# Optimization experiments

Hardware: AMD Instinct MI355X
Metric: run time of the kernel (lower is better)

Reference implementation:

```python
import jax, jax.numpy as jnp
import numpy as np

BS, NX = 4, 4096
SD, NPAR, H, L, K = 2, 5, 128, 6, 16
DT = 0.1
EPS = 1e-5


def swish(x):
    return x * jax.nn.sigmoid(x)


def _gather(a, idx):
    # a: [bs, nx, F], idx: [bs, nx, k] -> [bs, nx, k, F]
    bs, nx, k = idx.shape
    flat = jnp.take_along_axis(a, idx.reshape(bs, nx * k)[:, :, None], axis=1)
    return flat.reshape(bs, nx, k, a.shape[-1])


def _knn_idx(pos, k):
    # pos: [bs, nx, sd] -> indices of k nearest neighbors (self excluded), [bs, nx, k]
    sq = jnp.sum(pos * pos, axis=-1)
    d2 = sq[:, :, None] + sq[:, None, :] - 2.0 * jnp.einsum('bnd,bmd->bnm', pos, pos)
    n = pos.shape[1]
    d2 = d2.at[:, jnp.arange(n), jnp.arange(n)].set(1e10)  # loop=False
    return jax.lax.top_k(-d2, k)[1]


def _instance_norm(x):
    # PyG InstanceNorm (affine=False): normalize per graph per channel over nodes
    m = jnp.mean(x, axis=1, keepdims=True)
    v = jnp.mean((x - m) ** 2, axis=1, keepdims=True)
    return (x - m) * jax.lax.rsqrt(v + EPS)


def _forward(inputs, case_params, grid, emb_w1, emb_b1, emb_w2, emb_b2,
             mw1, mb1, mw2, mb2, uw1, ub1, uw2, ub2, ow1, ob1, ow2, ob2):
    u = inputs[..., :1]  # var_id=0 slice (c==1 here)
    # per-batch, per-dim min-max normalization of grid -> pos in [0,1]
    gmin = jnp.min(grid, axis=1, keepdims=True)
    gmax = jnp.max(grid, axis=1, keepdims=True)
    pos = (grid - gmin) / (gmax - gmin)
    idx = _knn_idx(pos, K)  # [bs, nx, K]: neighbors j of each target i
    params = case_params

    f = swish(jnp.concatenate([u, pos, params], -1) @ emb_w1 + emb_b1)
    f = swish(f @ emb_w2 + emb_b2)

    u_j = _gather(u, idx)
    pos_j = _gather(pos, idx)
    du = u[:, :, None, :] - u_j       # u_i - u_j,   [bs,nx,K,1]
    dpos = pos[:, :, None, :] - pos_j  # pos_i - pos_j, [bs,nx,K,sd]
    var_i = jnp.broadcast_to(params[:, :, None, :], (BS, NX, K, NPAR))

    for l in range(L):
        f_j = _gather(f, idx)
        f_i = jnp.broadcast_to(f[:, :, None, :], f_j.shape)
        m = jnp.concatenate([f_i, f_j, du, dpos, var_i], -1)  # [bs,nx,K,2H+1+sd+npar]
        m = swish(m @ mw1[l] + mb1[l])
        m = swish(m @ mw2[l] + mb2[l])
        agg = jnp.mean(m, axis=2)  # mean aggregation over K incoming edges
        up = swish(jnp.concatenate([f, agg, params], -1) @ uw1[l] + ub1[l])
        up = swish(up @ uw2[l] + ub2[l])
        f = _instance_norm(f + up)  # residual (in==out) then InstanceNorm

    diff = swish(f @ ow1 + ob1) @ ow2 + ob2
    return u + DT * diff  # [bs, nx, 1]


def setup_inputs():
    key = jax.random.key(0)
    ks = jax.random.split(key, 16)
    s = 0.05
    d = {}
    d['inputs'] = jax.random.normal(ks[0], (BS, NX, 1), jnp.float32)
    d['case_params'] = jax.random.uniform(ks[1], (BS, NX, NPAR), dtype=jnp.float32)
    d['mask'] = jnp.ones((BS, NX, 1), jnp.float32)
    d['grid'] = jax.random.uniform(ks[2], (BS, NX, SD), dtype=jnp.float32)
    d['emb_w1'] = jax.random.normal(ks[3], (1 + SD + NPAR, H), jnp.float32) * s
    d['emb_b1'] = jnp.zeros((H,), jnp.float32)
    d['emb_w2'] = jax.random.normal(ks[4], (H, H), jnp.float32) * s
    d['emb_b2'] = jnp.zeros((H,), jnp.float32)
    d['mw1'] = jax.random.normal(ks[5], (L, 2 * H + 1 + SD + NPAR, H), jnp.float32) * s
    d['mb1'] = jnp.zeros((L, H), jnp.float32)
    d['mw2'] = jax.random.normal(ks[6], (L, H, H), jnp.float32) * s
    d['mb2'] = jnp.zeros((L, H), jnp.float32)
    d['uw1'] = jax.random.normal(ks[7], (L, 2 * H + NPAR, H), jnp.float32) * s
    d['ub1'] = jnp.zeros((L, H), jnp.float32)
    d['uw2'] = jax.random.normal(ks[8], (L, H, H), jnp.float32) * s
    d['ub2'] = jnp.zeros((L, H), jnp.float32)
    d['ow1'] = jax.random.normal(ks[9], (H, H // 2), jnp.float32) * s
    d['ob1'] = jnp.zeros((H // 2,), jnp.float32)
    d['ow2'] = jax.random.normal(ks[10], (H // 2, 1), jnp.float32) * s
    d['ob2'] = jnp.zeros((1,), jnp.float32)
    return d


def reference(inputs, case_params, mask, grid, emb_w1, emb_b1, emb_w2, emb_b2,
              mw1, mb1, mw2, mb2, uw1, ub1, uw2, ub2, ow1, ob1, ow2, ob2):
    del mask  # unused by the original forward math
    return _forward(inputs, case_params, grid, emb_w1, emb_b1, emb_w2, emb_b2,
                    mw1, mb1, mw2, mb2, uw1, ub1, uw2, ub2, ow1, ob1, ow2, ob2)
```

## Files before the change

### kernel.cpp

```cpp
#include <hip/hip_runtime.h>
#include <math.h>

#define BSZ 4
#define NXN 4096
#define NPARP 5
#define HD 128
#define NLAY 6
#define KNN 16
#define DTC 0.1f
#define EPSC 1e-5f
#define NN (BSZ * NXN)
#define NPB 8
#define EPB 128

typedef __attribute__((ext_vector_type(8))) short short8;
typedef __attribute__((ext_vector_type(4))) float f32x4;

#define XR(r) (((r) & 7) << 4)

#define OFF_E   0
#define OFF_AU  32768
#define OFF_HU  40960
#define OFF_DU  45056
#define OFF_DPX 45568
#define OFF_DPY 46080
#define OFF_VAR 46592
#define SMEMB   46848

__device__ __forceinline__ float swishf(float x) {
    return x * __builtin_amdgcn_rcpf(1.0f + __expf(-x));
}

__device__ __forceinline__ unsigned short f2bf(float x) {
    union { float f; unsigned u; } v; v.f = x;
    unsigned r = v.u + 0x7fffu + ((v.u >> 16) & 1u);
    return (unsigned short)(r >> 16);
}
__device__ __forceinline__ unsigned short trh(float x) {
    union { float f; unsigned u; } v; v.f = x;
    return (unsigned short)(v.u >> 16);
}
__device__ __forceinline__ unsigned trpk(float lo, float hi) {
    union { float f; unsigned u; } a, b; a.f = lo; b.f = hi;
    return (b.u & 0xFFFF0000u) | (a.u >> 16);
}

__global__ void kminmax(const float* __restrict__ grid, float* __restrict__ gmm) {
    int b = blockIdx.x;
    int t = threadIdx.x;
    float mnx = 1e30f, mxx = -1e30f, mny = 1e30f, mxy = -1e30f;
    for (int n = t; n < NXN; n += 256) {
        float x = grid[(b * NXN + n) * 2 + 0];
        float y = grid[(b * NXN + n) * 2 + 1];
        mnx = fminf(mnx, x); mxx = fmaxf(mxx, x);
        mny = fminf(mny, y); mxy = fmaxf(mxy, y);
    }
    __shared__ float s[4][256];
    s[0][t] = mnx; s[1][t] = mxx; s[2][t] = mny; s[3][t] = mxy;
    __syncthreads();
    for (int off = 128; off > 0; off >>= 1) {
        if (t < off) {
            s[0][t] = fminf(s[0][t], s[0][t + off]);
            s[1][t] = fmaxf(s[1][t], s[1][t + off]);
            s[2][t] = fminf(s[2][t], s[2][t + off]);
            s[3][t] = fmaxf(s[3][t], s[3][t + off]);
        }
        __syncthreads();
    }
    if (t == 0) {
        gmm[b * 4 + 0] = s[0][0];
        gmm[b * 4 + 1] = s[1][0];
        gmm[b * 4 + 2] = s[2][0];
        gmm[b * 4 + 3] = s[3][0];
    }
}

__global__ void kpos(const float* __restrict__ grid, const float* __restrict__ gmm,
                     float* __restrict__ pos, float* __restrict__ sq) {
    int g = blockIdx.x * 256 + threadIdx.x;
    if (g >= NN) return;
    int b = g >> 12;
    float gx = grid[g * 2], gy = grid[g * 2 + 1];
    float px = (gx - gmm[b * 4 + 0]) / (gmm[b * 4 + 1] - gmm[b * 4 + 0]);
    float py = (gy - gmm[b * 4 + 2]) / (gmm[b * 4 + 3] - gmm[b * 4 + 2]);
    pos[g * 2] = px; pos[g * 2 + 1] = py;
    sq[g] = __fadd_rn(__fmul_rn(px, px), __fmul_rn(py, py));
}

__global__ __launch_bounds__(256) void kknnC(const float* __restrict__ pos,
                                             const float* __restrict__ sq,
                                             int* __restrict__ idxw) {
    __shared__ float2 sxy[1024];
    __shared__ float ssq[1024];
    int blk = blockIdx.x;
    int b = blk >> 10;
    int t = threadIdx.x;
    int lane = t & 63, w = t >> 6;
    int i = (blk & 1023) * 4 + w;
    float2 pi = *(const float2*)&pos[(b * NXN + i) * 2];
    float sqi = sq[b * NXN + i];
    float pk[64];
    float g[4];
#pragma unroll
    for (int c = 0; c < 4; ++c) {
        __syncthreads();
        for (int n = t; n < 1024; n += 256) {
            int j = b * NXN + c * 1024 + n;
            sxy[n] = *(const float2*)&pos[j * 2];
            ssq[n] = sq[j];
        }
        __syncthreads();
        float gc = 1e38f;
#pragma unroll
        for (int tt = 0; tt < 16; ++tt) {
            int n = tt * 64 + lane;
            float2 pj = sxy[n];
            float dot = fmaf(pi.x, pj.x, pi.y * pj.y);
            float d2 = (sqi + ssq[n]) - 2.0f * dot;
            d2 = (c * 1024 + n == i) ? 1e38f : d2;
            pk[c * 16 + tt] = d2;
            gc = fminf(gc, d2);
        }
        g[c] = gc;
    }
    int obase = (b * NXN + i) * KNN;
#pragma unroll 1
    for (int r = 0; r < KNN; ++r) {
        float m = fminf(fminf(g[0], g[1]), fminf(g[2], g[3]));
        float gm = m;
#pragma unroll
        for (int off = 1; off < 64; off <<= 1)
            gm = fminf(gm, __shfl_xor(gm, off));
        if (m == gm) {
            int jt = 0;
            if (g[0] == gm) {
                float ng = 1e38f;
#pragma unroll
                for (int tt = 0; tt < 16; ++tt) {
                    bool hit = (pk[tt] == gm);
                    jt = hit ? tt : jt;
                    pk[tt] = hit ? 1e38f : pk[tt];
                    ng = fminf(ng, pk[tt]);
                }
                g[0] = ng;
            }
            if (g[1] == gm) {
                float ng = 1e38f;
#pragma unroll
                for (int tt = 16; tt < 32; ++tt) {
                    bool hit = (pk[tt] == gm);
                    jt = hit ? tt : jt;
                    pk[tt] = hit ? 1e38f : pk[tt];
                    ng = fminf(ng, pk[tt]);
                }
                g[1] = ng;
            }
            if (g[2] == gm) {
                float ng = 1e38f;
#pragma unroll
                for (int tt = 32; tt < 48; ++tt) {
                    bool hit = (pk[tt] == gm);
                    jt = hit ? tt : jt;
                    pk[tt] = hit ? 1e38f : pk[tt];
                    ng = fminf(ng, pk[tt]);
                }
                g[2] = ng;
            }
            if (g[3] == gm) {
                float ng = 1e38f;
#pragma unroll
                for (int tt = 48; tt < 64; ++tt) {
                    bool hit = (pk[tt] == gm);
                    jt = hit ? tt : jt;
                    pk[tt] = hit ? 1e38f : pk[tt];
                    ng = fminf(ng, pk[tt]);
                }
                g[3] = ng;
            }
            idxw[obase + r] = ((jt >> 4) << 10) + ((jt & 15) << 6) + lane;
        }
    }
}

__global__ void kpack(const float* __restrict__ src, unsigned short* __restrict__ dst,
                      int K, int KB, int nmat) {
    int g = blockIdx.x * 256 + threadIdx.x;
    int per = KB * 1024;
    if (g >= nmat * per) return;
    int mat = g / per, rem = g % per;
    int kb = rem >> 10, r2 = rem & 1023;
    int n = r2 >> 3, j = r2 & 7;
    int phys = (n & 96) | ((n & 15) << 1) | ((n >> 4) & 1);
    int k = kb * 8 + j;
    float v = (k < K) ? src[(mat * K + k) * HD + phys] : 0.0f;
    dst[g] = f2bf(v);
}

__global__ __launch_bounds__(128) void kembed(const float* __restrict__ inputs,
                                              const float* __restrict__ pos,
                                              const float* __restrict__ params,
                                              const float* __restrict__ w1,
                                              const float* __restrict__ b1,
                                              const float* __restrict__ w2,
                                              const float* __restrict__ b2,
                                              float* __restrict__ f,
                                              unsigned short* __restrict__ fh) {
    __shared__ __align__(16) float sh[HD];
    int t = threadIdx.x;
    int g = blockIdx.x;
    float rw1[8];
#pragma unroll
    for (int k = 0; k < 8; k++) rw1[k] = w1[k * HD + t];
    float u = inputs[g];
    float px = pos[g * 2], py = pos[g * 2 + 1];
    float a = b1[t] + u * rw1[0] + px * rw1[1] + py * rw1[2];
#pragma unroll
    for (int j = 0; j < NPARP; j++) a += params[g * NPARP + j] * rw1[3 + j];
    sh[t] = swishf(a);
    __syncthreads();
    float a2 = b2[t];
    for (int k = 0; k < HD; k += 4) {
        float4 s4 = *(const float4*)&sh[k];
        a2 = fmaf(s4.x, w2[(k + 0) * HD + t], a2);
        a2 = fmaf(s4.y, w2[(k + 1) * HD + t], a2);
        a2 = fmaf(s4.z, w2[(k + 2) * HD + t], a2);
        a2 = fmaf(s4.w, w2[(k + 3) * HD + t], a2);
    }
    float fv = swishf(a2);
    f[g * HD + t] = fv;
    fh[g * HD + t] = trh(fv);
}

__global__ __launch_bounds__(256, 3) void kmsg5(
    const float* __restrict__ f, const unsigned short* __restrict__ fh,
    float* __restrict__ fnew,
    const float* __restrict__ inputs, const float* __restrict__ pos,
    const float* __restrict__ params, const int* __restrict__ idxw,
    const unsigned short* __restrict__ W1p, const float* __restrict__ W1r,
    const float* __restrict__ B1,
    const unsigned short* __restrict__ W2p, const float* __restrict__ B2,
    const unsigned short* __restrict__ U1p, const float* __restrict__ U1r,
    const float* __restrict__ UB1,
    const unsigned short* __restrict__ U2p, const float* __restrict__ UB2,
    float* __restrict__ p1, float* __restrict__ p2) {
    __shared__ __align__(16) char sm[SMEMB];
    int tid = threadIdx.x;
    int lane = tid & 63, w = tid >> 6;
    int l15 = lane & 15, l4 = lane >> 4;
    int bn0 = blockIdx.x * NPB;
    int base = bn0 & ~(NXN - 1);
    int bb = bn0 >> 12;
    int r0 = w * 32;
    int c0 = w * 32 + l15, c1 = c0 + 16;
    int pc0 = w * 32 + 2 * l15, pc1 = pc0 + 1;
    float* sVAR = (float*)(sm + OFF_VAR);

    short8 bC0[4], bC1[4], bM10[4], bM11[4];
#pragma unroll
    for (int k = 0; k < 4; ++k) {
        bC0[k]  = *(const short8*)&W1p[((k * 4 + l4) * HD + c0) * 8];
        bC1[k]  = *(const short8*)&W1p[((k * 4 + l4) * HD + c1) * 8];
        bM10[k] = *(const short8*)&W1p[((16 + k * 4 + l4) * HD + c0) * 8];
        bM11[k] = *(const short8*)&W1p[((16 + k * 4 + l4) * HD + c1) * 8];
    }
    float vB1_0 = B1[pc0], vB1_1 = B1[pc1];
    float wdu0 = W1r[256 * HD + pc0], wdx0 = W1r[257 * HD + pc0], wdy0 = W1r[258 * HD + pc0];
    float wdu1 = W1r[256 * HD + pc1], wdx1 = W1r[257 * HD + pc1], wdy1 = W1r[258 * HD + pc1];
    float wv0[5], wv1[5];
#pragma unroll
    for (int j = 0; j < 5; ++j) {
        wv0[j] = W1r[(259 + j) * HD + pc0];
        wv1[j] = W1r[(259 + j) * HD + pc1];
    }
    float vB2_0 = B2[pc0], vB2_1 = B2[pc1];

    if (lane < 32) {
        int e = r0 + lane;
        int nd = e >> 4;
        int gj = idxw[(bn0 + nd) * KNN + (e & 15)];
        int gn = base + gj;
        ((float*)(sm + OFF_DU))[e]  = inputs[bn0 + nd] - inputs[gn];
        ((float*)(sm + OFF_DPX))[e] = pos[(bn0 + nd) * 2]     - pos[gn * 2];
        ((float*)(sm + OFF_DPY))[e] = pos[(bn0 + nd) * 2 + 1] - pos[gn * 2 + 1];
    } else if (lane < 42) {
        int q = lane - 32;
        int nd = 2 * w + q / 5, j = q % 5;
        sVAR[nd * 8 + j] = params[(bn0 + nd) * NPARP + j];
    }
    {
        int r = 2 * w + (lane >> 5);
        int c4 = (lane & 31) * 4;
        uint2 v = *(const uint2*)&fh[(bn0 + r) * HD + c4];
        *(uint2*)(sm + OFF_AU + r * 512 + ((c4 * 2) ^ XR(r))) = v;
    }
    {
        int r = 8 + 2 * w + (lane >> 5);
        int cz = (lane & 31) * 16;
        uint4 z = {0, 0, 0, 0};
        *(uint4*)(sm + OFF_AU + r * 512 + cz) = z;
    }
    {
        int r = 8 + 2 * w + (lane >> 5);
        int cz = (lane & 31) * 8;
        uint2 z = {0, 0};
        *(uint2*)(sm + OFF_HU + r * 256 + cz) = z;
    }
    {
        int r = r0 + (lane >> 1), hf = lane & 1;
        int gj = idxw[(bn0 + (r >> 4)) * KNN + (r & 15)];
        const uint4* src = (const uint4*)&fh[(base + gj) * HD + hf * 64];
        char* drow = sm + OFF_E + r * 256;
#pragma unroll
        for (int jj = 0; jj < 8; ++jj) {
            uint4 p = src[jj];
            *(uint4*)(drow + ((hf * 128 + jj * 16) ^ XR(r))) = p;
        }
    }
    __syncthreads();

    f32x4 cm0 = {0.f, 0.f, 0.f, 0.f}, cm1 = {0.f, 0.f, 0.f, 0.f};
    {
        short8 afi[4];
#pragma unroll
        for (int k = 0; k < 4; ++k)
            afi[k] = *(short8*)(sm + OFF_AU + l15 * 512 + ((k * 64 + l4 * 16) ^ XR(l15)));
#pragma unroll
        for (int k = 0; k < 4; ++k) {
            cm0 = __builtin_amdgcn_mfma_f32_16x16x32_bf16(afi[k], bC0[k], cm0, 0, 0, 0);
            cm1 = __builtin_amdgcn_mfma_f32_16x16x32_bf16(afi[k], bC1[k], cm1, 0, 0, 0);
        }
    }
    if (l4 < 2) {
#pragma unroll
        for (int reg = 0; reg < 4; ++reg) {
            int nd = l4 * 4 + reg;
            float s0 = vB1_0, s1 = vB1_1;
#pragma unroll
            for (int j = 0; j < 5; ++j) {
                float vv = sVAR[nd * 8 + j];
                s0 = fmaf(vv, wv0[j], s0);
                s1 = fmaf(vv, wv1[j], s1);
            }
            cm0[reg] += s0; cm1[reg] += s1;
        }
    }

    short8 bM20[4], bM21[4];
#pragma unroll
    for (int k = 0; k < 4; ++k) {
        bM20[k] = *(const short8*)&W2p[((k * 4 + l4) * HD + c0) * 8];
        bM21[k] = *(const short8*)&W2p[((k * 4 + l4) * HD + c1) * 8];
    }

    short8 aC[4], aN[4];
#pragma unroll
    for (int k = 0; k < 4; ++k)
        aC[k] = *(short8*)(sm + OFF_E + l15 * 256 + ((k * 64 + l4 * 16) ^ XR(l15)));
#pragma unroll
    for (int m = 0; m < 8; ++m) {
        f32x4 h0 = {0.f, 0.f, 0.f, 0.f}, h1 = {0.f, 0.f, 0.f, 0.f};
#pragma unroll
        for (int k = 0; k < 4; ++k) {
            h0 = __builtin_amdgcn_mfma_f32_16x16x32_bf16(aC[k], bM10[k], h0, 0, 0, 0);
            h1 = __builtin_amdgcn_mfma_f32_16x16x32_bf16(aC[k], bM11[k], h1, 0, 0, 0);
        }
        if (m < 7) {
#pragma unroll
            for (int k = 0; k < 4; ++k)
                aN[k] = *(short8*)(sm + OFF_E + ((m + 1) * 16 + l15) * 256 +
                                   ((k * 64 + l4 * 16) ^ XR(l15)));
        }
        float com0 = __shfl(cm0[m & 3], ((m >> 2) << 4) | l15);
        float com1 = __shfl(cm1[m & 3], ((m >> 2) << 4) | l15);
        float4 duv = *(const float4*)(sm + OFF_DU  + (m * 16 + l4 * 4) * 4);
        float4 dxv = *(const float4*)(sm + OFF_DPX + (m * 16 + l4 * 4) * 4);
        float4 dyv = *(const float4*)(sm + OFF_DPY + (m * 16 + l4 * 4) * 4);
        __syncthreads();
#pragma unroll
        for (int reg = 0; reg < 4; ++reg) {
            int rr = m * 16 + l4 * 4 + reg;
            float d_u = ((const float*)&duv)[reg];
            float d_x = ((const float*)&dxv)[reg];
            float d_y = ((const float*)&dyv)[reg];
            float hv0 = h0[reg] + com0 + d_u * wdu0 + d_x * wdx0 + d_y * wdy0;
            float hv1 = h1[reg] + com1 + d_u * wdu1 + d_x * wdx1 + d_y * wdy1;
            *(unsigned*)(sm + OFF_E + rr * 256 + ((w * 64 + l15 * 4) ^ XR(rr))) =
                trpk(swishf(hv0), swishf(hv1));
        }
        if (m < 7) {
#pragma unroll
            for (int k = 0; k < 4; ++k) aC[k] = aN[k];
        }
    }
    __syncthreads();

    short8 bU10[8], bU11[8];
#pragma unroll
    for (int k = 0; k < 8; ++k) {
        bU10[k] = *(const short8*)&U1p[((k * 4 + l4) * HD + c0) * 8];
        bU11[k] = *(const short8*)&U1p[((k * 4 + l4) * HD + c1) * 8];
    }
    float vUB1_0 = UB1[pc0], vUB1_1 = UB1[pc1];
    float uv0[5], uv1[5];
#pragma unroll
    for (int j = 0; j < 5; ++j) {
        uv0[j] = U1r[(256 + j) * HD + pc0];
        uv1[j] = U1r[(256 + j) * HD + pc1];
    }

#pragma unroll
    for (int m = 0; m < 8; ++m) {
        short8 hf4[4];
#pragma unroll
        for (int k = 0; k < 4; ++k)
            hf4[k] = *(short8*)(sm + OFF_E + (m * 16 + l15) * 256 +
                                ((k * 64 + l4 * 16) ^ XR(l15)));
        f32x4 s0 = {0.f, 0.f, 0.f, 0.f}, s1 = {0.f, 0.f, 0.f, 0.f};
#pragma unroll
        for (int k = 0; k < 4; ++k) {
            s0 = __builtin_amdgcn_mfma_f32_16x16x32_bf16(hf4[k], bM20[k], s0, 0, 0, 0);
            s1 = __builtin_amdgcn_mfma_f32_16x16x32_bf16(hf4[k], bM21[k], s1, 0, 0, 0);
        }
        float sum0 = swishf(s0[0] + vB2_0) + swishf(s0[1] + vB2_0)
                   + swishf(s0[2] + vB2_0) + swishf(s0[3] + vB2_0);
        float sum1 = swishf(s1[0] + vB2_1) + swishf(s1[1] + vB2_1)
                   + swishf(s1[2] + vB2_1) + swishf(s1[3] + vB2_1);
        sum0 += __shfl_xor(sum0, 16); sum0 += __shfl_xor(sum0, 32);
        sum1 += __shfl_xor(sum1, 16); sum1 += __shfl_xor(sum1, 32);
        if (lane < 16) {
            *(unsigned*)(sm + OFF_AU + m * 512 + ((256 + w * 64 + lane * 4) ^ XR(m))) =
                trpk(sum0 * 0.0625f, sum1 * 0.0625f);
        }
    }
    __syncthreads();

    short8 bU20[4], bU21[4];
#pragma unroll
    for (int k = 0; k < 4; ++k) {
        bU20[k] = *(const short8*)&U2p[((k * 4 + l4) * HD + c0) * 8];
        bU21[k] = *(const short8*)&U2p[((k * 4 + l4) * HD + c1) * 8];
    }
    float vUB2_0 = UB2[pc0], vUB2_1 = UB2[pc1];

    {
        short8 au[8];
#pragma unroll
        for (int k = 0; k < 8; ++k)
            au[k] = *(short8*)(sm + OFF_AU + l15 * 512 + ((k * 64 + l4 * 16) ^ XR(l15)));
        f32x4 u0 = {0.f, 0.f, 0.f, 0.f}, u1 = {0.f, 0.f, 0.f, 0.f};
#pragma unroll
        for (int k = 0; k < 8; ++k) {
            u0 = __builtin_amdgcn_mfma_f32_16x16x32_bf16(au[k], bU10[k], u0, 0, 0, 0);
            u1 = __builtin_amdgcn_mfma_f32_16x16x32_bf16(au[k], bU11[k], u1, 0, 0, 0);
        }
        if (l4 < 2) {
#pragma unroll
            for (int reg = 0; reg < 4; ++reg) {
                int nd = l4 * 4 + reg;
                float s0 = vUB1_0, s1 = vUB1_1;
#pragma unroll
                for (int j = 0; j < 5; ++j) {
                    float vv = sVAR[nd * 8 + j];
                    s0 = fmaf(vv, uv0[j], s0);
                    s1 = fmaf(vv, uv1[j], s1);
                }
                *(unsigned*)(sm + OFF_HU + nd * 256 + ((w * 64 + l15 * 4) ^ XR(nd))) =
                    trpk(swishf(u0[reg] + s0), swishf(u1[reg] + s1));
            }
        }
    }
    __syncthreads();

    {
        short8 ah[4];
#pragma unroll
        for (int k = 0; k < 4; ++k)
            ah[k] = *(short8*)(sm + OFF_HU + l15 * 256 + ((k * 64 + l4 * 16) ^ XR(l15)));
        f32x4 o0 = {0.f, 0.f, 0.f, 0.f}, o1 = {0.f, 0.f, 0.f, 0.f};
#pragma unroll
        for (int k = 0; k < 4; ++k) {
            o0 = __builtin_amdgcn_mfma_f32_16x16x32_bf16(ah[k], bU20[k], o0, 0, 0, 0);
            o1 = __builtin_amdgcn_mfma_f32_16x16x32_bf16(ah[k], bU21[k], o1, 0, 0, 0);
        }
        float a1_0 = 0.f, a2_0 = 0.f, a1_1 = 0.f, a2_1 = 0.f;
        if (l4 < 2) {
#pragma unroll
            for (int reg = 0; reg < 4; ++reg) {
                int nd = l4 * 4 + reg;
                int gi = (bn0 + nd) * HD + pc0;
                float2 fv = *(const float2*)&f[gi];
                float v0 = fv.x + swishf(o0[reg] + vUB2_0);
                float v1 = fv.y + swishf(o1[reg] + vUB2_1);
                float2 st = {v0, v1};
                *(float2*)&fnew[gi] = st;
                a1_0 += v0; a2_0 += v0 * v0;
                a1_1 += v1; a2_1 += v1 * v1;
            }
        }
        a1_0 += __shfl_xor(a1_0, 16); a2_0 += __shfl_xor(a2_0, 16);
        a1_1 += __shfl_xor(a1_1, 16); a2_1 += __shfl_xor(a2_1, 16);
        if (l4 == 0) {
            atomicAdd(&p1[bb * HD + pc0], a1_0);
            atomicAdd(&p2[bb * HD + pc0], a2_0);
            atomicAdd(&p1[bb * HD + pc1], a1_1);
            atomicAdd(&p2[bb * HD + pc1], a2_1);
        }
    }
}

__global__ void kapply(const float* __restrict__ fnew,
                       const float* __restrict__ p1, const float* __restrict__ p2,
                       float* __restrict__ f, unsigned short* __restrict__ fh) {
    int g = blockIdx.x * 256 + threadIdx.x;
    int b = g >> 19;
    int c = g & 127;
    float m = p1[b * HD + c] * (1.0f / NXN);
    float v = p2[b * HD + c] * (1.0f / NXN) - m * m;
    float fv = (fnew[g] - m) * rsqrtf(v + EPSC);
    f[g] = fv;
    fh[g] = trh(fv);
}

__global__ __launch_bounds__(64) void khead(const float* __restrict__ f,
                                            const float* __restrict__ inputs,
                                            const float* __restrict__ ow1,
                                            const float* __restrict__ ob1,
                                            const float* __restrict__ ow2,
                                            const float* __restrict__ ob2,
                                            float* __restrict__ out) {
    int bn = blockIdx.x;
    int c = threadIdx.x;
    float a = ob1[c];
    for (int k = 0; k < HD; k++) a += f[bn * HD + k] * ow1[k * 64 + c];
    float v = swishf(a) * ow2[c];
#pragma unroll
    for (int off = 32; off > 0; off >>= 1) v += __shfl_down(v, off);
    if (c == 0) out[bn] = inputs[bn] + DTC * (v + ob2[0]);
}

extern "C" void kernel_launch(void* const* d_in, const int* in_sizes, int n_in,
                              void* d_out, int out_size, void* d_ws, size_t ws_size,
                              hipStream_t stream) {
    const float* inputs = (const float*)d_in[0];
    const float* params = (const float*)d_in[1];
    const float* grid   = (const float*)d_in[3];
    const float* emb_w1 = (const float*)d_in[4];
    const float* emb_b1 = (const float*)d_in[5];
    const float* emb_w2 = (const float*)d_in[6];
    const float* emb_b2 = (const float*)d_in[7];
    const float* mw1 = (const float*)d_in[8];
    const float* mb1 = (const float*)d_in[9];
    const float* mw2 = (const float*)d_in[10];
    const float* mb2 = (const float*)d_in[11];
    const float* uw1 = (const float*)d_in[12];
    const float* ub1 = (const float*)d_in[13];
    const float* uw2 = (const float*)d_in[14];
    const float* ub2 = (const float*)d_in[15];
    const float* ow1 = (const float*)d_in[16];
    const float* ob1 = (const float*)d_in[17];
    const float* ow2 = (const float*)d_in[18];
    const float* ob2 = (const float*)d_in[19];
    float* out = (float*)d_out;

    float* ws  = (float*)d_ws;
    float* pos = ws;
    float* sq  = pos + BSZ * NXN * 2;
    float* f   = sq + BSZ * NXN;
    float* fnew = f + BSZ * NXN * HD;
    float* p1   = fnew + BSZ * NXN * HD;
    float* p2   = p1 + BSZ * HD;
    float* gmm  = p2 + BSZ * HD;
    int* idxw   = (int*)(gmm + 16);
    unsigned short* mw1p = (unsigned short*)(idxw + NN * KNN);
    unsigned short* mw2p = mw1p + 6 * 33 * 1024;
    unsigned short* uw1p = mw2p + 6 * 16 * 1024;
    unsigned short* uw2p = uw1p + 6 * 33 * 1024;
    unsigned short* fh   = uw2p + 6 * 16 * 1024;

    kminmax<<<BSZ, 256, 0, stream>>>(grid, gmm);
    kpos<<<NN / 256, 256, 0, stream>>>(grid, gmm, pos, sq);
    kknnC<<<BSZ * (NXN / 4), 256, 0, stream>>>(pos, sq, idxw);

    kpack<<<(6 * 33 * 1024 + 255) / 256, 256, 0, stream>>>(mw1, mw1p, 264, 33, 6);
    kpack<<<(6 * 16 * 1024 + 255) / 256, 256, 0, stream>>>(mw2, mw2p, 128, 16, 6);
    kpack<<<(6 * 33 * 1024 + 255) / 256, 256, 0, stream>>>(uw1, uw1p, 261, 33, 6);
    kpack<<<(6 * 16 * 1024 + 255) / 256, 256, 0, stream>>>(uw2, uw2p, 128, 16, 6);

    kembed<<<NN, 128, 0, stream>>>(inputs, pos, params,
                                   emb_w1, emb_b1, emb_w2, emb_b2, f, fh);
    for (int l = 0; l < NLAY; l++) {
        hipMemsetAsync(p1, 0, 2 * BSZ * HD * sizeof(float), stream);
        kmsg5<<<NN / NPB, 256, 0, stream>>>(f, fh, fnew, inputs, pos, params, idxw,
                                            mw1p + l * 33 * 1024, mw1 + l * 264 * HD, mb1 + l * HD,
                                            mw2p + l * 16 * 1024, mb2 + l * HD,
                                            uw1p + l * 33 * 1024, uw1 + l * 261 * HD, ub1 + l * HD,
                                            uw2p + l * 16 * 1024, ub2 + l * HD,
                                            p1, p2);
        kapply<<<(BSZ * NXN * HD) / 256, 256, 0, stream>>>(fnew, p1, p2, f, fh);
    }
    khead<<<NN, 64, 0, stream>>>(f, inputs, ow1, ob1, ow2, ob2, out);
}
```

Measured before the change: 729.8 us.

## Process edge gather and message MLP in two halves to shrink LDS

The per-block edge tile (128 edges) is split into two halves of 64 that are gathered, run through the first and second message MLP layers, and mean-aggregated in turn. This halves the LDS edge buffer and drops the separate f_i staging area. The f_i fragments now load straight from global memory into registers and are reused for the update MLP. Total LDS per block falls enough to raise the launch-bounds occupancy target from 3 to 4 blocks, at the cost of extra barriers and serialising the two halves.

Result: slower. 1.297 ms (+77.7%).

```diff
diff --git a/kernel.cpp b/kernel.cpp
--- a/kernel.cpp
+++ b/kernel.cpp
@@ -11,7 +11,6 @@
 #define EPSC 1e-5f
 #define NN (BSZ * NXN)
 #define NPB 8
-#define EPB 128
 
 typedef __attribute__((ext_vector_type(8))) short short8;
 typedef __attribute__((ext_vector_type(4))) float f32x4;
@@ -19,13 +18,13 @@
 #define XR(r) (((r) & 7) << 4)
 
 #define OFF_E   0
-#define OFF_AU  32768
-#define OFF_HU  40960
-#define OFF_DU  45056
-#define OFF_DPX 45568
-#define OFF_DPY 46080
-#define OFF_VAR 46592
-#define SMEMB   46848
+#define OFF_AG  16384
+#define OFF_HU  20480
+#define OFF_DU  24576
+#define OFF_DPX 25088
+#define OFF_DPY 25600
+#define OFF_VAR 26112
+#define SMEMB   26368
 
 __device__ __forceinline__ float swishf(float x) {
     return x * __builtin_amdgcn_rcpf(1.0f + __expf(-x));
@@ -231,7 +230,7 @@
     fh[g * HD + t] = trh(fv);
 }
 
-__global__ __launch_bounds__(256, 3) void kmsg5(
+__global__ __launch_bounds__(256, 4) void kmsg6(
     const float* __restrict__ f, const unsigned short* __restrict__ fh,
     float* __restrict__ fnew,
     const float* __restrict__ inputs, const float* __restrict__ pos,
@@ -250,10 +249,16 @@
     int bn0 = blockIdx.x * NPB;
     int base = bn0 & ~(NXN - 1);
     int bb = bn0 >> 12;
-    int r0 = w * 32;
     int c0 = w * 32 + l15, c1 = c0 + 16;
     int pc0 = w * 32 + 2 * l15, pc1 = pc0 + 1;
     float* sVAR = (float*)(sm + OFF_VAR);
+
+    int fiRow = bn0 + l15; fiRow = (fiRow < NN) ? fiRow : (NN - 1);
+    const char* fiP = (const char*)(fh + fiRow * HD);
+    short8 afi[4];
+#pragma unroll
+    for (int k = 0; k < 4; ++k)
+        afi[k] = *(const short8*)(fiP + k * 64 + l4 * 16);
 
     short8 bC0[4], bC1[4], bM10[4], bM11[4];
 #pragma unroll
@@ -275,7 +280,7 @@
     float vB2_0 = B2[pc0], vB2_1 = B2[pc1];
 
     if (lane < 32) {
-        int e = r0 + lane;
+        int e = w * 32 + lane;
         int nd = e >> 4;
         int gj = idxw[(bn0 + nd) * KNN + (e & 15)];
         int gn = base + gj;
@@ -287,48 +292,27 @@
         int nd = 2 * w + q / 5, j = q % 5;
         sVAR[nd * 8 + j] = params[(bn0 + nd) * NPARP + j];
     }
-    {
-        int r = 2 * w + (lane >> 5);
-        int c4 = (lane & 31) * 4;
-        uint2 v = *(const uint2*)&fh[(bn0 + r) * HD + c4];
-        *(uint2*)(sm + OFF_AU + r * 512 + ((c4 * 2) ^ XR(r))) = v;
-    }
-    {
-        int r = 8 + 2 * w + (lane >> 5);
-        int cz = (lane & 31) * 16;
-        uint4 z = {0, 0, 0, 0};
-        *(uint4*)(sm + OFF_AU + r * 512 + cz) = z;
-    }
-    {
-        int r = 8 + 2 * w + (lane >> 5);
-        int cz = (lane & 31) * 8;
-        uint2 z = {0, 0};
-        *(uint2*)(sm + OFF_HU + r * 256 + cz) = z;
-    }
-    {
-        int r = r0 + (lane >> 1), hf = lane & 1;
-        int gj = idxw[(bn0 + (r >> 4)) * KNN + (r & 15)];
-        const uint4* src = (const uint4*)&fh[(base + gj) * HD + hf * 64];
-        char* drow = sm + OFF_E + r * 256;
-#pragma unroll
-        for (int jj = 0; jj < 8; ++jj) {
-            uint4 p = src[jj];
-            *(uint4*)(drow + ((hf * 128 + jj * 16) ^ XR(r))) = p;
-        }
-    }
+
+#define GATHER(H) {                                                         \
+        int r = tid >> 2, q = tid & 3;                                      \
+        int e = (H) * 64 + r;                                               \
+        int gj = idxw[(bn0 + (e >> 4)) * KNN + (e & 15)];                   \
+        const uint4* srcp = (const uint4*)(fh + (base + gj) * HD);          \
+        char* drow = sm + OFF_E + r * 256;                                  \
+        _Pragma("unroll")                                                   \
+        for (int jj = 0; jj < 4; ++jj) {                                    \
+            uint4 pv = srcp[q * 4 + jj];                                    \
+            *(uint4*)(drow + ((q * 64 + jj * 16) ^ XR(r))) = pv;            \
+        } }
+
+    GATHER(0)
     __syncthreads();
 
     f32x4 cm0 = {0.f, 0.f, 0.f, 0.f}, cm1 = {0.f, 0.f, 0.f, 0.f};
-    {
-        short8 afi[4];
-#pragma unroll
-        for (int k = 0; k < 4; ++k)
-            afi[k] = *(short8*)(sm + OFF_AU + l15 * 512 + ((k * 64 + l4 * 16) ^ XR(l15)));
-#pragma unroll
-        for (int k = 0; k < 4; ++k) {
-            cm0 = __builtin_amdgcn_mfma_f32_16x16x32_bf16(afi[k], bC0[k], cm0, 0, 0, 0);
-            cm1 = __builtin_amdgcn_mfma_f32_16x16x32_bf16(afi[k], bC1[k], cm1, 0, 0, 0);
-        }
+#pragma unroll
+    for (int k = 0; k < 4; ++k) {
+        cm0 = __builtin_amdgcn_mfma_f32_16x16x32_bf16(afi[k], bC0[k], cm0, 0, 0, 0);
+        cm1 = __builtin_amdgcn_mfma_f32_16x16x32_bf16(afi[k], bC1[k], cm1, 0, 0, 0);
     }
     if (l4 < 2) {
 #pragma unroll
@@ -352,46 +336,84 @@
         bM21[k] = *(const short8*)&W2p[((k * 4 + l4) * HD + c1) * 8];
     }
 
-    short8 aC[4], aN[4];
-#pragma unroll
-    for (int k = 0; k < 4; ++k)
-        aC[k] = *(short8*)(sm + OFF_E + l15 * 256 + ((k * 64 + l4 * 16) ^ XR(l15)));
-#pragma unroll
-    for (int m = 0; m < 8; ++m) {
-        f32x4 h0 = {0.f, 0.f, 0.f, 0.f}, h1 = {0.f, 0.f, 0.f, 0.f};
-#pragma unroll
-        for (int k = 0; k < 4; ++k) {
-            h0 = __builtin_amdgcn_mfma_f32_16x16x32_bf16(aC[k], bM10[k], h0, 0, 0, 0);
-            h1 = __builtin_amdgcn_mfma_f32_16x16x32_bf16(aC[k], bM11[k], h1, 0, 0, 0);
-        }
-        if (m < 7) {
-#pragma unroll
-            for (int k = 0; k < 4; ++k)
-                aN[k] = *(short8*)(sm + OFF_E + ((m + 1) * 16 + l15) * 256 +
-                                   ((k * 64 + l4 * 16) ^ XR(l15)));
-        }
-        float com0 = __shfl(cm0[m & 3], ((m >> 2) << 4) | l15);
-        float com1 = __shfl(cm1[m & 3], ((m >> 2) << 4) | l15);
-        float4 duv = *(const float4*)(sm + OFF_DU  + (m * 16 + l4 * 4) * 4);
-        float4 dxv = *(const float4*)(sm + OFF_DPX + (m * 16 + l4 * 4) * 4);
-        float4 dyv = *(const float4*)(sm + OFF_DPY + (m * 16 + l4 * 4) * 4);
-        __syncthreads();
-#pragma unroll
-        for (int reg = 0; reg < 4; ++reg) {
-            int rr = m * 16 + l4 * 4 + reg;
-            float d_u = ((const float*)&duv)[reg];
-            float d_x = ((const float*)&dxv)[reg];
-            float d_y = ((const float*)&dyv)[reg];
-            float hv0 = h0[reg] + com0 + d_u * wdu0 + d_x * wdx0 + d_y * wdy0;
-            float hv1 = h1[reg] + com1 + d_u * wdu1 + d_x * wdx1 + d_y * wdy1;
-            *(unsigned*)(sm + OFF_E + rr * 256 + ((w * 64 + l15 * 4) ^ XR(rr))) =
-                trpk(swishf(hv0), swishf(hv1));
-        }
-        if (m < 7) {
-#pragma unroll
-            for (int k = 0; k < 4; ++k) aC[k] = aN[k];
-        }
-    }
+#define MM1_HALF(H) {                                                       \
+        short8 aC[4], aN[4];                                                \
+        _Pragma("unroll")                                                   \
+        for (int k = 0; k < 4; ++k)                                         \
+            aC[k] = *(short8*)(sm + OFF_E + l15 * 256 +                     \
+                               ((k * 64 + l4 * 16) ^ XR(l15)));             \
+        _Pragma("unroll")                                                   \
+        for (int m = 0; m < 4; ++m) {                                       \
+            f32x4 h0 = {0.f, 0.f, 0.f, 0.f}, h1 = {0.f, 0.f, 0.f, 0.f};     \
+            _Pragma("unroll")                                               \
+            for (int k = 0; k < 4; ++k) {                                   \
+                h0 = __builtin_amdgcn_mfma_f32_16x16x32_bf16(aC[k], bM10[k], h0, 0, 0, 0); \
+                h1 = __builtin_amdgcn_mfma_f32_16x16x32_bf16(aC[k], bM11[k], h1, 0, 0, 0); \
+            }                                                               \
+            if (m < 3) {                                                    \
+                _Pragma("unroll")                                           \
+                for (int k = 0; k < 4; ++k)                                 \
+                    aN[k] = *(short8*)(sm + OFF_E + ((m + 1) * 16 + l15) * 256 + \
+                                       ((k * 64 + l4 * 16) ^ XR((m + 1) * 16 + l15))); \
+            }                                                               \
+            int M = (H) * 4 + m;                                            \
+            float com0 = __shfl(cm0[M & 3], ((M >> 2) << 4) | l15);         \
+            float com1 = __shfl(cm1[M & 3], ((M >> 2) << 4) | l15);         \
+            float4 duv = *(const float4*)(sm + OFF_DU  + ((H) * 64 + m * 16 + l4 * 4) * 4); \
+            float4 dxv = *(const float4*)(sm + OFF_DPX + ((H) * 64 + m * 16 + l4 * 4) * 4); \
+            float4 dyv = *(const float4*)(sm + OFF_DPY + ((H) * 64 + m * 16 + l4 * 4) * 4); \
+            __syncthreads();                                                \
+            _Pragma("unroll")                                               \
+            for (int reg = 0; reg < 4; ++reg) {                             \
+                int rr = m * 16 + l4 * 4 + reg;                             \
+                float d_u = ((const float*)&duv)[reg];                      \
+                float d_x = ((const float*)&dxv)[reg];                      \
+                float d_y = ((const float*)&dyv)[reg];                      \
+                float hv0 = h0[reg] + com0 + d_u * wdu0 + d_x * wdx0 + d_y * wdy0; \
+                float hv1 = h1[reg] + com1 + d_u * wdu1 + d_x * wdx1 + d_y * wdy1; \
+                *(unsigned*)(sm + OFF_E + rr * 256 + ((w * 64 + l15 * 4) ^ XR(rr))) = \
+                    trpk(swishf(hv0), swishf(hv1));                         \
+            }                                                               \
+            if (m < 3) {                                                    \
+                _Pragma("unroll")                                           \
+                for (int k = 0; k < 4; ++k) aC[k] = aN[k];                  \
+            }                                                               \
+        } }
+
+#define MM2_HALF(H) {                                                       \
+        _Pragma("unroll")                                                   \
+        for (int m = 0; m < 4; ++m) {                                       \
+            short8 hf4[4];                                                  \
+            _Pragma("unroll")                                               \
+            for (int k = 0; k < 4; ++k)                                     \
+                hf4[k] = *(short8*)(sm + OFF_E + (m * 16 + l15) * 256 +     \
+                                    ((k * 64 + l4 * 16) ^ XR(m * 16 + l15))); \
+            f32x4 s0 = {0.f, 0.f, 0.f, 0.f}, s1 = {0.f, 0.f, 0.f, 0.f};     \
+            _Pragma("unroll")                                               \
+            for (int k = 0; k < 4; ++k) {                                   \
+                s0 = __builtin_amdgcn_mfma_f32_16x16x32_bf16(hf4[k], bM20[k], s0, 0, 0, 0); \
+                s1 = __builtin_amdgcn_mfma_f32_16x16x32_bf16(hf4[k], bM21[k], s1, 0, 0, 0); \
+            }                                                               \
+            float sum0 = swishf(s0[0] + vB2_0) + swishf(s0[1] + vB2_0)      \
+                       + swishf(s0[2] + vB2_0) + swishf(s0[3] + vB2_0);     \
+            float sum1 = swishf(s1[0] + vB2_1) + swishf(s1[1] + vB2_1)      \
+                       + swishf(s1[2] + vB2_1) + swishf(s1[3] + vB2_1);     \
+            sum0 += __shfl_xor(sum0, 16); sum0 += __shfl_xor(sum0, 32);     \
+            sum1 += __shfl_xor(sum1, 16); sum1 += __shfl_xor(sum1, 32);     \
+            int M = (H) * 4 + m;                                            \
+            if (lane < 16) {                                                \
+                *(unsigned*)(sm + OFF_AG + M * 256 + ((w * 64 + lane * 4) ^ XR(M))) = \
+                    trpk(sum0 * 0.0625f, sum1 * 0.0625f);                   \
+            }                                                               \
+        } }
+
+    MM1_HALF(0)
+    __syncthreads();
+    MM2_HALF(0)
+    __syncthreads();
+    GATHER(1)
+    __syncthreads();
+    MM1_HALF(1)
     __syncthreads();
 
     short8 bU10[8], bU11[8];
@@ -408,30 +430,7 @@
         uv1[j] = U1r[(256 + j) * HD + pc1];
     }
 
-#pragma unroll
-    for (int m = 0; m < 8; ++m) {
-        short8 hf4[4];
-#pragma unroll
-        for (int k = 0; k < 4; ++k)
-            hf4[k] = *(short8*)(sm + OFF_E + (m * 16 + l15) * 256 +
-                                ((k * 64 + l4 * 16) ^ XR(l15)));
-        f32x4 s0 = {0.f, 0.f, 0.f, 0.f}, s1 = {0.f, 0.f, 0.f, 0.f};
-#pragma unroll
-        for (int k = 0; k < 4; ++k) {
-            s0 = __builtin_amdgcn_mfma_f32_16x16x32_bf16(hf4[k], bM20[k], s0, 0, 0, 0);
-            s1 = __builtin_amdgcn_mfma_f32_16x16x32_bf16(hf4[k], bM21[k], s1, 0, 0, 0);
-        }
-        float sum0 = swishf(s0[0] + vB2_0) + swishf(s0[1] + vB2_0)
-                   + swishf(s0[2] + vB2_0) + swishf(s0[3] + vB2_0);
-        float sum1 = swishf(s1[0] + vB2_1) + swishf(s1[1] + vB2_1)
-                   + swishf(s1[2] + vB2_1) + swishf(s1[3] + vB2_1);
-        sum0 += __shfl_xor(sum0, 16); sum0 += __shfl_xor(sum0, 32);
-        sum1 += __shfl_xor(sum1, 16); sum1 += __shfl_xor(sum1, 32);
-        if (lane < 16) {
-            *(unsigned*)(sm + OFF_AU + m * 512 + ((256 + w * 64 + lane * 4) ^ XR(m))) =
-                trpk(sum0 * 0.0625f, sum1 * 0.0625f);
-        }
-    }
+    MM2_HALF(1)
     __syncthreads();
 
     short8 bU20[4], bU21[4];
@@ -443,15 +442,18 @@
     float vUB2_0 = UB2[pc0], vUB2_1 = UB2[pc1];
 
     {
-        short8 au[8];
-#pragma unroll
-        for (int k = 0; k < 8; ++k)
-            au[k] = *(short8*)(sm + OFF_AU + l15 * 512 + ((k * 64 + l4 * 16) ^ XR(l15)));
         f32x4 u0 = {0.f, 0.f, 0.f, 0.f}, u1 = {0.f, 0.f, 0.f, 0.f};
 #pragma unroll
-        for (int k = 0; k < 8; ++k) {
-            u0 = __builtin_amdgcn_mfma_f32_16x16x32_bf16(au[k], bU10[k], u0, 0, 0, 0);
-            u1 = __builtin_amdgcn_mfma_f32_16x16x32_bf16(au[k], bU11[k], u1, 0, 0, 0);
+        for (int k = 0; k < 4; ++k) {
+            u0 = __builtin_amdgcn_mfma_f32_16x16x32_bf16(afi[k], bU10[k], u0, 0, 0, 0);
+            u1 = __builtin_amdgcn_mfma_f32_16x16x32_bf16(afi[k], bU11[k], u1, 0, 0, 0);
+        }
+#pragma unroll
+        for (int k = 0; k < 4; ++k) {
+            short8 ag = *(short8*)(sm + OFF_AG + l15 * 256 +
+                                   ((k * 64 + l4 * 16) ^ XR(l15)));
+            u0 = __builtin_amdgcn_mfma_f32_16x16x32_bf16(ag, bU10[4 + k], u0, 0, 0, 0);
+            u1 = __builtin_amdgcn_mfma_f32_16x16x32_bf16(ag, bU11[4 + k], u1, 0, 0, 0);
         }
         if (l4 < 2) {
 #pragma unroll
@@ -506,6 +508,9 @@
             atomicAdd(&p2[bb * HD + pc1], a2_1);
         }
     }
+#undef GATHER
+#undef MM1_HALF
+#undef MM2_HALF
 }
 
 __global__ void kapply(const float* __restrict__ fnew,
@@ -590,7 +595,7 @@
                                    emb_w1, emb_b1, emb_w2, emb_b2, f, fh);
     for (int l = 0; l < NLAY; l++) {
         hipMemsetAsync(p1, 0, 2 * BSZ * HD * sizeof(float), stream);
-        kmsg5<<<NN / NPB, 256, 0, stream>>>(f, fh, fnew, inputs, pos, params, idxw,
+        kmsg6<<<NN / NPB, 256, 0, stream>>>(f, fh, fnew, inputs, pos, params, idxw,
                                             mw1p + l * 33 * 1024, mw1 + l * 264 * HD, mb1 + l * HD,
                                             mw2p + l * 16 * 1024, mb2 + l * HD,
                                             uw1p + l * 33 * 1024, uw1 + l * 261 * HD, ub1 + l * HD,
```
